# Optimization experiments

Hardware: AMD Instinct MI355X
Metric: run time of the kernel (lower is better)

Reference implementation:

```python
import jax, jax.numpy as jnp
import numpy as np
import math

MAX_L = 3
N_NODES, N_RADIAL, N_CHANNEL = 50000, 8, 16


def _build_tables(max_l):
    # Cartesian angular basis (lx,ly,lz) with lx+ly+lz <= max_l, (0,0,0) first.
    l_list = []
    for l in range(max_l + 1):
        for lx in range(l, -1, -1):
            for ly in range(l - lx, -1, -1):
                l_list.append((lx, ly, l - lx - ly))
    idx = {t: i for i, t in enumerate(l_list)}
    # nu=2 combos: per l (slot l-1), sum of multinomial-weighted squares.
    indices, pref, slots = [], [], []
    for l in range(1, max_l + 1):
        for lx in range(l, -1, -1):
            for ly in range(l - lx, -1, -1):
                lz = l - lx - ly
                i = idx[(lx, ly, lz)]
                indices.append([i, i])
                pref.append(math.factorial(l) / (math.factorial(lx) * math.factorial(ly) * math.factorial(lz)))
                slots.append(l - 1)
    return (np.asarray(indices, np.int32), np.asarray(pref, np.float32),
            np.asarray(slots, np.int32), len(l_list))


def setup_inputs() -> dict:
    key = jax.random.key(0)
    indices, pref, slots, n_ang = _build_tables(MAX_L)
    node_attr = jax.random.normal(key, (N_NODES, N_RADIAL, n_ang, N_CHANNEL), dtype=jnp.float32)
    return {
        "node_attr": node_attr,
        "prefactors": jnp.asarray(pref),
        "indices": jnp.asarray(indices),
        "slots": jnp.asarray(slots),
    }


def reference(node_attr, prefactors, indices, slots):
    # node_attr: [N, R, A, C]; indices: [M, 2]; prefactors: [M]; slots: [M]
    n, r, _, c = node_attr.shape
    n_slots = MAX_L  # one slot per order l for nu=2
    g = node_attr[:, :, indices, :]                    # [N, R, M, 2, C] gather
    prod = g[..., 0, :] * g[..., 1, :]                 # product over nu dim
    weighted = prod * prefactors[None, None, :, None]  # prefactor scale
    sym_rest = jnp.zeros((n, r, n_slots, c), node_attr.dtype)
    sym_rest = sym_rest.at[:, :, slots, :].add(weighted)  # scatter_add into slots
    # slot 0 is the raw l=0 channel
    return jnp.concatenate([node_attr[:, :, :1, :], sym_rest], axis=2)
```

## Files before the change

kernel.cpp:

```cpp
#include <hip/hip_runtime.h>


typedef float f32x4 __attribute__((ext_vector_type(4)));

constexpr int ROWS_PB     = 64;
constexpr int IN_ROW_F4   = 80;
constexpr int OUT_ROW_F4  = 16;
constexpr int STAGE_F4    = 76;
constexpr int LDS_STRIDE_DW = 308;
constexpr int LOADS_PT    = (ROWS_PB * STAGE_F4) / 256;

__global__ __launch_bounds__(256) void symmetrizer_kernel(
    const f32x4* __restrict__ in,
    f32x4*       __restrict__ out)
{
    extern __shared__ float lds[];

    const int t = threadIdx.x;
    const size_t base_f4 = (size_t)blockIdx.x * ROWS_PB * IN_ROW_F4;

    f32x4 g[LOADS_PT];
    unsigned rr[LOADS_PT], ww[LOADS_PT];
#pragma unroll
    for (int i = 0; i < LOADS_PT; ++i) {
        unsigned f = (unsigned)(i * 256 + t);
        unsigned r = f / STAGE_F4;
        unsigned w = f - r * STAGE_F4;
        rr[i] = r; ww[i] = w;
        g[i] = in[base_f4 + r * IN_ROW_F4 + 4 + w];
    }
#pragma unroll
    for (int i = 0; i < LOADS_PT; ++i) {
        *(f32x4*)&lds[rr[i] * LDS_STRIDE_DW + ww[i] * 4] = g[i];
    }

    const int r  = t >> 2;
    const int c4 = t & 3;

    f32x4 v0 = in[base_f4 + (size_t)r * IN_ROW_F4 + c4];

    __syncthreads();

    const int rb = r * LDS_STRIDE_DW + c4 * 4;
    f32x4 d[19];
#pragma unroll
    for (int k = 0; k < 19; ++k) {
        d[k] = *(const f32x4*)&lds[rb + k * 16];
    }

    f32x4 s0 = d[0] * d[0] + d[1] * d[1] + d[2] * d[2];

    f32x4 s1 = d[3] * d[3] + 2.f * (d[4] * d[4]) + 2.f * (d[5] * d[5])
             + d[6] * d[6] + 2.f * (d[7] * d[7]) + d[8] * d[8];

    f32x4 s2 = d[9] * d[9]  + 3.f * (d[10] * d[10]) + 3.f * (d[11] * d[11])
             + 3.f * (d[12] * d[12]) + 6.f * (d[13] * d[13])
             + 3.f * (d[14] * d[14]) + d[15] * d[15]
             + 3.f * (d[16] * d[16]) + 3.f * (d[17] * d[17])
             + d[18] * d[18];

    f32x4* ob = out + ((size_t)blockIdx.x * ROWS_PB + r) * OUT_ROW_F4 + c4;
    __builtin_nontemporal_store(v0, ob + 0);
    __builtin_nontemporal_store(s0, ob + 4);
    __builtin_nontemporal_store(s1, ob + 8);
    __builtin_nontemporal_store(s2, ob + 12);
}

extern "C" void kernel_launch(void* const* d_in, const int* in_sizes, int n_in,
                              void* d_out, int out_size, void* d_ws, size_t ws_size,
                              hipStream_t stream) {
    const float* node_attr = (const float*)d_in[0];
    float*       out       = (float*)d_out;

    int rows   = in_sizes[0] / (20 * 16);
    int blocks = rows / ROWS_PB;
    size_t lds_bytes = ROWS_PB * LDS_STRIDE_DW * sizeof(float);

    symmetrizer_kernel<<<blocks, 256, lds_bytes, stream>>>(
        (const f32x4*)node_attr, (f32x4*)out);
}
```

Baseline: 110.7 us.

## Use persistent single-wave blocks with double-buffered direct global-to-LDS loads

```diff
diff --git a/kernel.cpp b/kernel.cpp
--- a/kernel.cpp
+++ b/kernel.cpp
@@ -3,67 +3,98 @@
 
 typedef float f32x4 __attribute__((ext_vector_type(4)));
 
-constexpr int ROWS_PB     = 64;
-constexpr int IN_ROW_F4   = 80;
-constexpr int OUT_ROW_F4  = 16;
-constexpr int STAGE_F4    = 76;
-constexpr int LDS_STRIDE_DW = 308;
-constexpr int LOADS_PT    = (ROWS_PB * STAGE_F4) / 256;
+constexpr int ROWS_PT      = 16;
+constexpr int IN_ROW_F4    = 80;
+constexpr int OUT_ROW_F4   = 16;
+constexpr int STAGE_F4     = 76;
+constexpr int TILE_F4      = ROWS_PT * STAGE_F4;
+constexpr int GLL_PER_TILE = TILE_F4 / 64;
+constexpr int BUF_DW       = TILE_F4 * 4;
+constexpr int GRID_BLOCKS  = 1024;
 
-__global__ __launch_bounds__(256) void symmetrizer_kernel(
-    const f32x4* __restrict__ in,
-    f32x4*       __restrict__ out)
+__device__ __forceinline__ void gload_lds16(const float* g, float* l) {
+    __builtin_amdgcn_global_load_lds(
+        (const __attribute__((address_space(1))) void*)g,
+        (__attribute__((address_space(3))) void*)l,
+        16, 0, 0);
+}
+
+__global__ __launch_bounds__(64) void symmetrizer_kernel(
+    const float* __restrict__ in,
+    f32x4*       __restrict__ out,
+    int n_tiles)
 {
     extern __shared__ float lds[];
-
-    const int t = threadIdx.x;
-    const size_t base_f4 = (size_t)blockIdx.x * ROWS_PB * IN_ROW_F4;
-
-    f32x4 g[LOADS_PT];
-    unsigned rr[LOADS_PT], ww[LOADS_PT];
-#pragma unroll
-    for (int i = 0; i < LOADS_PT; ++i) {
-        unsigned f = (unsigned)(i * 256 + t);
-        unsigned r = f / STAGE_F4;
-        unsigned w = f - r * STAGE_F4;
-        rr[i] = r; ww[i] = w;
-        g[i] = in[base_f4 + r * IN_ROW_F4 + 4 + w];
-    }
-#pragma unroll
-    for (int i = 0; i < LOADS_PT; ++i) {
-        *(f32x4*)&lds[rr[i] * LDS_STRIDE_DW + ww[i] * 4] = g[i];
-    }
-
+    const int t  = threadIdx.x;
     const int r  = t >> 2;
     const int c4 = t & 3;
 
-    f32x4 v0 = in[base_f4 + (size_t)r * IN_ROW_F4 + c4];
+    int tile = blockIdx.x;
+    int cur  = 0;
 
-    __syncthreads();
+    {
+        const float* gb = in + (size_t)tile * ROWS_PT * IN_ROW_F4 * 4;
+#pragma unroll
+        for (int i = 0; i < GLL_PER_TILE; ++i) {
+            unsigned f  = i * 64 + t;
+            unsigned rr = f / STAGE_F4;
+            unsigned jj = f - rr * STAGE_F4;
+            gload_lds16(gb + (rr * IN_ROW_F4 + 4u + jj) * 4u,
+                        &lds[i * 256]);
+        }
+    }
+    f32x4 v0c = *(const f32x4*)(in +
+        ((size_t)(tile * ROWS_PT + r) * IN_ROW_F4 + c4) * 4);
 
-    const int rb = r * LDS_STRIDE_DW + c4 * 4;
-    f32x4 d[19];
+    while (true) {
+        const int  next     = tile + GRID_BLOCKS;
+        const bool has_next = next < n_tiles;
+        f32x4 v0n;
+
+        if (has_next) {
+            const float* gb = in + (size_t)next * ROWS_PT * IN_ROW_F4 * 4;
 #pragma unroll
-    for (int k = 0; k < 19; ++k) {
-        d[k] = *(const f32x4*)&lds[rb + k * 16];
+            for (int i = 0; i < GLL_PER_TILE; ++i) {
+                unsigned f  = i * 64 + t;
+                unsigned rr = f / STAGE_F4;
+                unsigned jj = f - rr * STAGE_F4;
+                gload_lds16(gb + (rr * IN_ROW_F4 + 4u + jj) * 4u,
+                            &lds[(cur ^ 1) * BUF_DW + i * 256]);
+            }
+            v0n = *(const f32x4*)(in +
+                ((size_t)(next * ROWS_PT + r) * IN_ROW_F4 + c4) * 4);
+            asm volatile("s_waitcnt vmcnt(20)" ::: "memory");
+        } else {
+            asm volatile("s_waitcnt vmcnt(0)" ::: "memory");
+        }
+        __builtin_amdgcn_sched_barrier(0);
+
+        const float* lb = &lds[cur * BUF_DW + r * (STAGE_F4 * 4) + c4 * 4];
+        f32x4 d[19];
+#pragma unroll
+        for (int k = 0; k < 19; ++k)
+            d[k] = *(const f32x4*)(lb + k * 16);
+
+        f32x4 s0 = d[0] * d[0] + d[1] * d[1] + d[2] * d[2];
+        f32x4 s1 = d[3] * d[3] + 2.f * (d[4] * d[4]) + 2.f * (d[5] * d[5])
+                 + d[6] * d[6] + 2.f * (d[7] * d[7]) + d[8] * d[8];
+        f32x4 s2 = d[9] * d[9]   + 3.f * (d[10] * d[10]) + 3.f * (d[11] * d[11])
+                 + 3.f * (d[12] * d[12]) + 6.f * (d[13] * d[13])
+                 + 3.f * (d[14] * d[14]) + d[15] * d[15]
+                 + 3.f * (d[16] * d[16]) + d[18] * d[18]
+                 + 3.f * (d[17] * d[17]);
+
+        f32x4* ob = out + (size_t)(tile * ROWS_PT + r) * OUT_ROW_F4 + c4;
+        __builtin_nontemporal_store(v0c, ob + 0);
+        __builtin_nontemporal_store(s0,  ob + 4);
+        __builtin_nontemporal_store(s1,  ob + 8);
+        __builtin_nontemporal_store(s2,  ob + 12);
+
+        if (!has_next) break;
+        v0c = v0n;
+        tile = next;
+        cur ^= 1;
     }
-
-    f32x4 s0 = d[0] * d[0] + d[1] * d[1] + d[2] * d[2];
-
-    f32x4 s1 = d[3] * d[3] + 2.f * (d[4] * d[4]) + 2.f * (d[5] * d[5])
-             + d[6] * d[6] + 2.f * (d[7] * d[7]) + d[8] * d[8];
-
-    f32x4 s2 = d[9] * d[9]  + 3.f * (d[10] * d[10]) + 3.f * (d[11] * d[11])
-             + 3.f * (d[12] * d[12]) + 6.f * (d[13] * d[13])
-             + 3.f * (d[14] * d[14]) + d[15] * d[15]
-             + 3.f * (d[16] * d[16]) + 3.f * (d[17] * d[17])
-             + d[18] * d[18];
-
-    f32x4* ob = out + ((size_t)blockIdx.x * ROWS_PB + r) * OUT_ROW_F4 + c4;
-    __builtin_nontemporal_store(v0, ob + 0);
-    __builtin_nontemporal_store(s0, ob + 4);
-    __builtin_nontemporal_store(s1, ob + 8);
-    __builtin_nontemporal_store(s2, ob + 12);
 }
 
 extern "C" void kernel_launch(void* const* d_in, const int* in_sizes, int n_in,
@@ -72,10 +103,10 @@
     const float* node_attr = (const float*)d_in[0];
     float*       out       = (float*)d_out;
 
-    int rows   = in_sizes[0] / (20 * 16);
-    int blocks = rows / ROWS_PB;
-    size_t lds_bytes = ROWS_PB * LDS_STRIDE_DW * sizeof(float);
+    int rows    = in_sizes[0] / (20 * 16);
+    int n_tiles = rows / ROWS_PT;
+    size_t lds_bytes = 2 * BUF_DW * sizeof(float);
 
-    symmetrizer_kernel<<<blocks, 256, lds_bytes, stream>>>(
-        (const f32x4*)node_attr, (f32x4*)out);
+    symmetrizer_kernel<<<GRID_BLOCKS, 64, lds_bytes, stream>>>(
+        node_attr, (f32x4*)out, n_tiles);
 }
```

New measurement: 112.6 us. Within noise of the previous version (+1.8%).
